# Optimization experiments

Measured on AMD Instinct MI355X. Metric: run time of the kernel, lower is better.

The kernel has to match this reference:

```python
import jax, jax.numpy as jnp
import numpy as np

B, N, D = 8, 1024, 1024
E, H = 16, 4096
CAP_FACTOR = 1.25  # training-mode capacity factor
NUM_CLASSES = 345


def setup_inputs() -> dict:
    key = jax.random.key(0)
    k1, k2, k3, k4 = jax.random.split(key, 4)
    inputs = jax.random.normal(k1, (B, N, D), dtype=jnp.float32)
    current_y = jax.random.randint(k2, (B,), 0, NUM_CLASSES, dtype=jnp.int32)
    std1 = 1.0 / np.sqrt(H)  # init_ uses 1/sqrt(last dim)
    std2 = 1.0 / np.sqrt(D)
    w1 = jax.random.uniform(k3, (E, D, H), dtype=jnp.float32, minval=-std1, maxval=std1)
    w2 = jax.random.uniform(k4, (E, H, D), dtype=jnp.float32, minval=-std2, maxval=std2)
    return {"inputs": inputs, "current_y": current_y, "w1": w1, "w2": w2}


def reference(inputs, current_y, w1, w2):
    b, n, d = inputs.shape
    e = w1.shape[0]
    cap = max(min(n, int(n * CAP_FACTOR / e)), 4)  # MIN_EXPERT_CAPACITY=4
    dt = inputs.dtype

    # class-based gating: every token of sample i goes to expert y_i % e
    idx = jnp.broadcast_to(jnp.remainder(current_y, e)[:, None], (b, n))  # (b,n)
    oh = jax.nn.one_hot(idx, e, dtype=dt)                                 # (b,n,e)
    # exclusive cumsum over token dim, masked
    pos = (jnp.cumsum(oh, axis=-2) - oh) * oh                             # (b,n,e)
    mask1 = oh * (pos < cap).astype(dt)                                   # drop overflow tokens
    mask1_flat = mask1.sum(axis=-1)                                       # (b,n)
    pos_flat = pos.sum(axis=-1).astype(jnp.int32)                         # (b,n)

    # combine[b,n,e,c]; out-of-range positions -> zero row (safe_one_hot semantics)
    combine = (mask1_flat[..., None, None]
               * oh[..., None]
               * jax.nn.one_hot(pos_flat, cap, dtype=dt)[..., None, :])
    dispatch = (combine > 0).astype(dt)

    # dispatch tokens to padded expert slots: (e, b, cap, d)
    expert_in = jnp.einsum('bnd,bnec->ebcd', inputs, dispatch).reshape(e, b * cap, d)
    hidden = jax.nn.gelu(jnp.einsum('end,edh->enh', expert_in, w1), approximate=False)
    expert_out = jnp.einsum('enh,ehd->end', hidden, w2).reshape(e, b, cap, d)

    output = jnp.einsum('ebcd,bnec->bnd', expert_out, combine)
    return output
```

## Files before the change

### kernel.cpp

```cpp
#include <hip/hip_runtime.h>
#include <hip/hip_bf16.h>

#define NB   8
#define NTOK 1024
#define DDIM 1024
#define NEXP 16
#define HDIM 4096
#define CAP  80
#define BK   64

using bf16x8 = __attribute__((ext_vector_type(8))) __bf16;
using bf16x4 = __attribute__((ext_vector_type(4))) __bf16;
using f32x4  = __attribute__((ext_vector_type(4))) float;

__global__ __launch_bounds__(256) void moe_g1(
    const float* __restrict__ X, const int* __restrict__ Y,
    const float* __restrict__ W1, __bf16* __restrict__ Hid)
{
    const int b     = blockIdx.y;
    const int e     = Y[b] & (NEXP - 1);
    const int nbase = blockIdx.x * 64;
    const int tid   = threadIdx.x;
    const int w     = tid >> 6;
    const int l     = tid & 63;
    const int q     = l >> 4;
    const int r     = l & 15;
    const int n     = nbase + w * 16 + r;

    __shared__ __bf16 As[CAP][BK + 8];

    const float* Xb  = X  + (size_t)b * NTOK * DDIM;
    const float* W1e = W1 + (size_t)e * DDIM * HDIM;

    f32x4 acc[5];
    #pragma unroll
    for (int i = 0; i < 5; ++i) acc[i] = f32x4{0.f, 0.f, 0.f, 0.f};

    for (int k0 = 0; k0 < DDIM; k0 += BK) {
        float bv[16];
        const float* bp = W1e + (size_t)(k0 + q * 8) * HDIM + n;
        #pragma unroll
        for (int s = 0; s < 2; ++s)
            #pragma unroll
            for (int j = 0; j < 8; ++j)
                bv[s * 8 + j] = bp[(size_t)(s * 32 + j) * HDIM];

        __syncthreads();
        #pragma unroll
        for (int it = 0; it < 5; ++it) {
            int i   = tid + 256 * it;
            int row = i >> 4, kg = i & 15;
            float4 v = *(const float4*)&Xb[(size_t)row * DDIM + k0 + kg * 4];
            bf16x4 p = {(__bf16)v.x, (__bf16)v.y, (__bf16)v.z, (__bf16)v.w};
            *(bf16x4*)&As[row][kg * 4] = p;
        }
        __syncthreads();

        #pragma unroll
        for (int s = 0; s < 2; ++s) {
            bf16x8 bf;
            #pragma unroll
            for (int j = 0; j < 8; ++j) bf[j] = (__bf16)bv[s * 8 + j];
            #pragma unroll
            for (int mt = 0; mt < 5; ++mt) {
                bf16x8 af = *(const bf16x8*)&As[mt * 16 + r][s * 32 + q * 8];
                acc[mt] = __builtin_amdgcn_mfma_f32_16x16x32_bf16(af, bf, acc[mt], 0, 0, 0);
            }
        }
    }

    __bf16* Hb = Hid + (size_t)b * CAP * HDIM;
    #pragma unroll
    for (int mt = 0; mt < 5; ++mt)
        #pragma unroll
        for (int v = 0; v < 4; ++v) {
            int m = mt * 16 + q * 4 + v;
            float x = acc[mt][v];
            float g = 0.5f * x * (1.0f + erff(x * 0.70710678118654752f));
            Hb[(size_t)m * HDIM + n] = (__bf16)g;
        }
}

__global__ __launch_bounds__(256) void moe_g2(
    const __bf16* __restrict__ Hid, const int* __restrict__ Y,
    const float* __restrict__ W2, float* __restrict__ Out)
{
    const int b     = blockIdx.y;
    const int e     = Y[b] & (NEXP - 1);
    const int nbase = blockIdx.x * 64;
    const int kz    = blockIdx.z * (HDIM / 4);
    const int tid   = threadIdx.x;
    const int w     = tid >> 6;
    const int l     = tid & 63;
    const int q     = l >> 4;
    const int r     = l & 15;
    const int n     = nbase + w * 16 + r;

    __shared__ __bf16 As[CAP][BK + 8];

    const __bf16* Hb  = Hid + (size_t)b * CAP * HDIM;
    const float*  W2e = W2  + (size_t)e * HDIM * DDIM;

    f32x4 acc[5];
    #pragma unroll
    for (int i = 0; i < 5; ++i) acc[i] = f32x4{0.f, 0.f, 0.f, 0.f};

    for (int k0 = kz; k0 < kz + HDIM / 4; k0 += BK) {
        float bv[16];
        const float* bp = W2e + (size_t)(k0 + q * 8) * DDIM + n;
        #pragma unroll
        for (int s = 0; s < 2; ++s)
            #pragma unroll
            for (int j = 0; j < 8; ++j)
                bv[s * 8 + j] = bp[(size_t)(s * 32 + j) * DDIM];

        __syncthreads();
        #pragma unroll
        for (int it = 0; it < 5; ++it) {
            int i   = tid + 256 * it;
            int row = i >> 4, kg = i & 15;
            uint2 v = *(const uint2*)&Hb[(size_t)row * HDIM + k0 + kg * 4];
            *(uint2*)&As[row][kg * 4] = v;
        }
        __syncthreads();

        #pragma unroll
        for (int s = 0; s < 2; ++s) {
            bf16x8 bf;
            #pragma unroll
            for (int j = 0; j < 8; ++j) bf[j] = (__bf16)bv[s * 8 + j];
            #pragma unroll
            for (int mt = 0; mt < 5; ++mt) {
                bf16x8 af = *(const bf16x8*)&As[mt * 16 + r][s * 32 + q * 8];
                acc[mt] = __builtin_amdgcn_mfma_f32_16x16x32_bf16(af, bf, acc[mt], 0, 0, 0);
            }
        }
    }

    float* Ob = Out + (size_t)b * NTOK * DDIM;
    #pragma unroll
    for (int mt = 0; mt < 5; ++mt)
        #pragma unroll
        for (int v = 0; v < 4; ++v) {
            int m = mt * 16 + q * 4 + v;
            atomicAdd(&Ob[(size_t)m * DDIM + n], acc[mt][v]);
        }
}

extern "C" void kernel_launch(void* const* d_in, const int* in_sizes, int n_in,
                              void* d_out, int out_size, void* d_ws, size_t ws_size,
                              hipStream_t stream) {
    const float* X  = (const float*)d_in[0];
    const int*   Y  = (const int*)d_in[1];
    const float* W1 = (const float*)d_in[2];
    const float* W2 = (const float*)d_in[3];
    float*  Out = (float*)d_out;
    __bf16* Hid = (__bf16*)d_ws;

    hipMemsetAsync(d_out, 0, (size_t)out_size * sizeof(float), stream);

    moe_g1<<<dim3(HDIM / 64, NB), 256, 0, stream>>>(X, Y, W1, Hid);
    moe_g2<<<dim3(DDIM / 64, NB, 4), 256, 0, stream>>>(Hid, Y, W2, Out);
}
```

Measured before the change: 472.3 us.

## Pre-convert tokens to bf16, drop LDS staging, register-prefetch next weight tile

Adds a small kernel that converts the first CAP tokens of each batch to bf16 once, so the GEMM kernels no longer repeat that conversion. Both GEMMs now read A fragments straight from global memory instead of staging them through shared memory, which removes the __syncthreads barriers. The next K-tile of weights is prefetched into registers while MFMAs run on the current one. The cost is an extra kernel launch and more registers, and A rows are reloaded redundantly by each wave from cache.

Measured after the change: 512.6 us. +8.5%, slower.

```diff
diff --git a/kernel.cpp b/kernel.cpp
--- a/kernel.cpp
+++ b/kernel.cpp
@@ -7,65 +7,84 @@
 #define NEXP 16
 #define HDIM 4096
 #define CAP  80
-#define BK   64
 
 using bf16x8 = __attribute__((ext_vector_type(8))) __bf16;
-using bf16x4 = __attribute__((ext_vector_type(4))) __bf16;
 using f32x4  = __attribute__((ext_vector_type(4))) float;
 
+__global__ __launch_bounds__(256) void cvt_x(
+    const float* __restrict__ X, __bf16* __restrict__ Xb)
+{
+    int t   = blockIdx.x * 256 + threadIdx.x;
+    int row = t >> 8;
+    int c4  = (t & 255) * 4;
+    int b   = row / CAP;
+    int m   = row - b * CAP;
+    float4 v = *(const float4*)&X[(size_t)b * NTOK * DDIM + (size_t)m * DDIM + c4];
+    bf16x8 dummy;
+    __bf16* dst = Xb + (size_t)row * DDIM + c4;
+    dst[0] = (__bf16)v.x; dst[1] = (__bf16)v.y; dst[2] = (__bf16)v.z; dst[3] = (__bf16)v.w;
+    (void)dummy;
+}
+
 __global__ __launch_bounds__(256) void moe_g1(
-    const float* __restrict__ X, const int* __restrict__ Y,
+    const __bf16* __restrict__ Xb, const int* __restrict__ Y,
     const float* __restrict__ W1, __bf16* __restrict__ Hid)
 {
-    const int b     = blockIdx.y;
-    const int e     = Y[b] & (NEXP - 1);
-    const int nbase = blockIdx.x * 64;
-    const int tid   = threadIdx.x;
-    const int w     = tid >> 6;
-    const int l     = tid & 63;
-    const int q     = l >> 4;
-    const int r     = l & 15;
-    const int n     = nbase + w * 16 + r;
+    const int b   = blockIdx.y;
+    const int e   = Y[b] & (NEXP - 1);
+    const int tid = threadIdx.x;
+    const int w   = tid >> 6, l = tid & 63, q = l >> 4, r = l & 15;
+    const int n   = blockIdx.x * 64 + w * 16 + r;
 
-    __shared__ __bf16 As[CAP][BK + 8];
-
-    const float* Xb  = X  + (size_t)b * NTOK * DDIM;
-    const float* W1e = W1 + (size_t)e * DDIM * HDIM;
+    const float*  Wb = W1 + (size_t)e * DDIM * HDIM + n;
+    const __bf16* Ab = Xb + (size_t)b * CAP * DDIM;
 
     f32x4 acc[5];
     #pragma unroll
     for (int i = 0; i < 5; ++i) acc[i] = f32x4{0.f, 0.f, 0.f, 0.f};
 
-    for (int k0 = 0; k0 < DDIM; k0 += BK) {
-        float bv[16];
-        const float* bp = W1e + (size_t)(k0 + q * 8) * HDIM + n;
+    float bcur[16];
+    #pragma unroll
+    for (int s = 0; s < 2; ++s)
+        #pragma unroll
+        for (int j = 0; j < 8; ++j)
+            bcur[s * 8 + j] = Wb[(size_t)(s * 32 + q * 8 + j) * HDIM];
+
+    #pragma unroll
+    for (int k0 = 0; k0 < DDIM; k0 += 64) {
+        bf16x8 af[2][5];
+        #pragma unroll
+        for (int s = 0; s < 2; ++s)
+            #pragma unroll
+            for (int mt = 0; mt < 5; ++mt)
+                af[s][mt] = *(const bf16x8*)&Ab[(size_t)(mt * 16 + r) * DDIM + k0 + s * 32 + q * 8];
+
+        float bnxt[16];
+        if (k0 + 64 < DDIM) {
+            const float* wp = Wb + (size_t)(k0 + 64) * HDIM;
+            #pragma unroll
+            for (int s = 0; s < 2; ++s)
+                #pragma unroll
+                for (int j = 0; j < 8; ++j)
+                    bnxt[s * 8 + j] = wp[(size_t)(s * 32 + q * 8 + j) * HDIM];
+        }
+
+        bf16x8 bf[2];
         #pragma unroll
         for (int s = 0; s < 2; ++s)
             #pragma unroll
             for (int j = 0; j < 8; ++j)
-                bv[s * 8 + j] = bp[(size_t)(s * 32 + j) * HDIM];
-
-        __syncthreads();
-        #pragma unroll
-        for (int it = 0; it < 5; ++it) {
-            int i   = tid + 256 * it;
-            int row = i >> 4, kg = i & 15;
-            float4 v = *(const float4*)&Xb[(size_t)row * DDIM + k0 + kg * 4];
-            bf16x4 p = {(__bf16)v.x, (__bf16)v.y, (__bf16)v.z, (__bf16)v.w};
-            *(bf16x4*)&As[row][kg * 4] = p;
-        }
-        __syncthreads();
+                bf[s][j] = (__bf16)bcur[s * 8 + j];
 
         #pragma unroll
-        for (int s = 0; s < 2; ++s) {
-            bf16x8 bf;
+        for (int s = 0; s < 2; ++s)
             #pragma unroll
-            for (int j = 0; j < 8; ++j) bf[j] = (__bf16)bv[s * 8 + j];
+            for (int mt = 0; mt < 5; ++mt)
+                acc[mt] = __builtin_amdgcn_mfma_f32_16x16x32_bf16(af[s][mt], bf[s], acc[mt], 0, 0, 0);
+
+        if (k0 + 64 < DDIM) {
             #pragma unroll
-            for (int mt = 0; mt < 5; ++mt) {
-                bf16x8 af = *(const bf16x8*)&As[mt * 16 + r][s * 32 + q * 8];
-                acc[mt] = __builtin_amdgcn_mfma_f32_16x16x32_bf16(af, bf, acc[mt], 0, 0, 0);
-            }
+            for (int i = 0; i < 16; ++i) bcur[i] = bnxt[i];
         }
     }
 
@@ -85,55 +104,63 @@
     const __bf16* __restrict__ Hid, const int* __restrict__ Y,
     const float* __restrict__ W2, float* __restrict__ Out)
 {
-    const int b     = blockIdx.y;
-    const int e     = Y[b] & (NEXP - 1);
-    const int nbase = blockIdx.x * 64;
-    const int kz    = blockIdx.z * (HDIM / 4);
-    const int tid   = threadIdx.x;
-    const int w     = tid >> 6;
-    const int l     = tid & 63;
-    const int q     = l >> 4;
-    const int r     = l & 15;
-    const int n     = nbase + w * 16 + r;
+    const int b   = blockIdx.y;
+    const int e   = Y[b] & (NEXP - 1);
+    const int kz  = blockIdx.z * (HDIM / 4);
+    const int tid = threadIdx.x;
+    const int w   = tid >> 6, l = tid & 63, q = l >> 4, r = l & 15;
+    const int n   = blockIdx.x * 64 + w * 16 + r;
 
-    __shared__ __bf16 As[CAP][BK + 8];
-
-    const __bf16* Hb  = Hid + (size_t)b * CAP * HDIM;
-    const float*  W2e = W2  + (size_t)e * HDIM * DDIM;
+    const float*  Wb = W2  + (size_t)e * HDIM * DDIM + n;
+    const __bf16* Ab = Hid + (size_t)b * CAP * HDIM;
 
     f32x4 acc[5];
     #pragma unroll
     for (int i = 0; i < 5; ++i) acc[i] = f32x4{0.f, 0.f, 0.f, 0.f};
 
-    for (int k0 = kz; k0 < kz + HDIM / 4; k0 += BK) {
-        float bv[16];
-        const float* bp = W2e + (size_t)(k0 + q * 8) * DDIM + n;
+    float bcur[16];
+    #pragma unroll
+    for (int s = 0; s < 2; ++s)
+        #pragma unroll
+        for (int j = 0; j < 8; ++j)
+            bcur[s * 8 + j] = Wb[(size_t)(kz + s * 32 + q * 8 + j) * DDIM];
+
+    #pragma unroll
+    for (int kk = 0; kk < HDIM / 4; kk += 64) {
+        const int k0 = kz + kk;
+        bf16x8 af[2][5];
+        #pragma unroll
+        for (int s = 0; s < 2; ++s)
+            #pragma unroll
+            for (int mt = 0; mt < 5; ++mt)
+                af[s][mt] = *(const bf16x8*)&Ab[(size_t)(mt * 16 + r) * HDIM + k0 + s * 32 + q * 8];
+
+        float bnxt[16];
+        if (kk + 64 < HDIM / 4) {
+            const float* wp = Wb + (size_t)(k0 + 64) * DDIM;
+            #pragma unroll
+            for (int s = 0; s < 2; ++s)
+                #pragma unroll
+                for (int j = 0; j < 8; ++j)
+                    bnxt[s * 8 + j] = wp[(size_t)(s * 32 + q * 8 + j) * DDIM];
+        }
+
+        bf16x8 bf[2];
         #pragma unroll
         for (int s = 0; s < 2; ++s)
             #pragma unroll
             for (int j = 0; j < 8; ++j)
-                bv[s * 8 + j] = bp[(size_t)(s * 32 + j) * DDIM];
-
-        __syncthreads();
-        #pragma unroll
-        for (int it = 0; it < 5; ++it) {
-            int i   = tid + 256 * it;
-            int row = i >> 4, kg = i & 15;
-            uint2 v = *(const uint2*)&Hb[(size_t)row * HDIM + k0 + kg * 4];
-            *(uint2*)&As[row][kg * 4] = v;
-        }
-        __syncthreads();
+                bf[s][j] = (__bf16)bcur[s * 8 + j];
 
         #pragma unroll
-        for (int s = 0; s < 2; ++s) {
-            bf16x8 bf;
+        for (int s = 0; s < 2; ++s)
             #pragma unroll
-            for (int j = 0; j < 8; ++j) bf[j] = (__bf16)bv[s * 8 + j];
+            for (int mt = 0; mt < 5; ++mt)
+                acc[mt] = __builtin_amdgcn_mfma_f32_16x16x32_bf16(af[s][mt], bf[s], acc[mt], 0, 0, 0);
+
+        if (kk + 64 < HDIM / 4) {
             #pragma unroll
-            for (int mt = 0; mt < 5; ++mt) {
-                bf16x8 af = *(const bf16x8*)&As[mt * 16 + r][s * 32 + q * 8];
-                acc[mt] = __builtin_amdgcn_mfma_f32_16x16x32_bf16(af, bf, acc[mt], 0, 0, 0);
-            }
+            for (int i = 0; i < 16; ++i) bcur[i] = bnxt[i];
         }
     }
 
@@ -155,10 +182,11 @@
     const float* W1 = (const float*)d_in[2];
     const float* W2 = (const float*)d_in[3];
     float*  Out = (float*)d_out;
-    __bf16* Hid = (__bf16*)d_ws;
+    __bf16* Xb  = (__bf16*)d_ws;
+    __bf16* Hid = (__bf16*)((char*)d_ws + (2u << 20));
 
     hipMemsetAsync(d_out, 0, (size_t)out_size * sizeof(float), stream);
-
-    moe_g1<<<dim3(HDIM / 64, NB), 256, 0, stream>>>(X, Y, W1, Hid);
+    cvt_x<<<dim3(640), 256, 0, stream>>>(X, Xb);
+    moe_g1<<<dim3(HDIM / 64, NB), 256, 0, stream>>>(Xb, Y, W1, Hid);
     moe_g2<<<dim3(DDIM / 64, NB, 4), 256, 0, stream>>>(Hid, Y, W2, Out);
 }
```
